# Performance work log

Measured on AMD Instinct MI355X. Metric: run time of the kernel, lower is better.

Reference implementation:

```python
import jax, jax.numpy as jnp
import numpy as np
import math

B, T, D, La, Lr = 8, 128, 512, 2, 2
H = La + Lr
DK = D // H  # 128
DFF = 4 * D


def _gelu(x):
    # BERT tanh-approx GELU, matching the torch module exactly
    return 0.5 * x * (1.0 + jnp.tanh(math.sqrt(2.0 / math.pi) * (x + 0.044715 * x ** 3)))


def _ln(x, g, b, eps=1e-5):
    mu = jnp.mean(x, axis=-1, keepdims=True)
    var = jnp.mean((x - mu) ** 2, axis=-1, keepdims=True)
    return (x - mu) * jax.lax.rsqrt(var + eps) * g + b


def setup_inputs() -> dict:
    key = jax.random.key(0)
    ks = jax.random.split(key, 16)
    n = lambda k, s, sc=1.0: jax.random.normal(k, s, dtype=jnp.float32) * sc
    return {
        'x': n(ks[0], (B, T, D)),
        'mask': jnp.ones((B, 1, T, T), dtype=jnp.int32),
        'abs_kernel': n(ks[1], (La, B, T, D)),
        'rel_kernel': n(ks[2], (Lr, B, T, T, D)),
        'Wc': n(ks[3], (3, D, D), 0.02), 'bc': jnp.zeros((3, D), jnp.float32),
        'Wpq': n(ks[4], (La, D, DK), 0.02), 'bpq': jnp.zeros((La, DK), jnp.float32),
        'Wpk': n(ks[5], (La, D, DK), 0.02), 'bpk': jnp.zeros((La, DK), jnp.float32),
        'Wrk': n(ks[6], (Lr, D, DK), 0.02), 'brk': jnp.zeros((Lr, DK), jnp.float32),
        'rel_bias': n(ks[7], (Lr, DK), 0.02),
        'Wo': n(ks[8], (D, D), 0.02), 'bo': jnp.zeros((D,), jnp.float32),
        'W1': n(ks[9], (D, DFF), 0.02), 'b1': jnp.zeros((DFF,), jnp.float32),
        'W2': n(ks[10], (DFF, D), 0.02), 'b2': jnp.zeros((D,), jnp.float32),
        'ln1_g': jnp.ones((D,), jnp.float32), 'ln1_b': jnp.zeros((D,), jnp.float32),
        'ln2_g': jnp.ones((D,), jnp.float32), 'ln2_b': jnp.zeros((D,), jnp.float32),
    }


def _attention(h, mask, abs_kernel, rel_kernel, Wc, bc, Wpq, bpq, Wpk, bpk,
               Wrk, brk, rel_bias, Wo, bo):
    b, t = h.shape[0], h.shape[1]
    # content projections: [3,B,T,D] -> [3,B,H,T,DK]
    qkv = jnp.einsum('btd,cde->cbte', h, Wc) + bc[:, None, None, :]
    qkv = qkv.reshape(3, b, t, H, DK).transpose(0, 1, 3, 2, 4)
    q, k, v = qkv[0], qkv[1], qkv[2]
    # absolute-position heads
    Pq = jnp.einsum('abtd,ade->bate', abs_kernel, Wpq) + bpq[None, :, None, :]
    Pk = jnp.einsum('abtd,ade->bate', abs_kernel, Wpk) + bpk[None, :, None, :]
    abs_scores = jnp.einsum('blid,bljd->blij', q[:, :La] + Pq, k[:, :La] + Pk)
    # relative-position heads (R: [B,Lr,T,T,DK])
    R = jnp.einsum('abijd,ade->baije', rel_kernel, Wrk) + brk[None, :, None, None, :]
    Xq = q[:, La:]
    rel_scores = jnp.einsum('blid,bljd->blij', Xq, k[:, La:])
    rel_scores = rel_scores + jnp.einsum('blid,blijd->blij', Xq + rel_bias[None, :, None, :], R)
    scores = jnp.concatenate([abs_scores, rel_scores], axis=1) * (DK ** -0.5)
    scores = jnp.where(mask == 0, jnp.float32(-1e9), scores)
    p_attn = jax.nn.softmax(scores, axis=-1)
    out = jnp.einsum('bhij,bhjd->bhid', p_attn, v)
    out = out.transpose(0, 2, 1, 3).reshape(b, t, H * DK)
    return out @ Wo + bo


def reference(x, mask, abs_kernel, rel_kernel, Wc, bc, Wpq, bpq, Wpk, bpk,
              Wrk, brk, rel_bias, Wo, bo, W1, b1, W2, b2,
              ln1_g, ln1_b, ln2_g, ln2_b):
    # pre-LN sublayer 1: attention
    h = _ln(x, ln1_g, ln1_b)
    x = x + _attention(h, mask, abs_kernel, rel_kernel, Wc, bc, Wpq, bpq,
                       Wpk, bpk, Wrk, brk, rel_bias, Wo, bo)
    # pre-LN sublayer 2: FFN with tanh-GELU
    h2 = _ln(x, ln2_g, ln2_b)
    x = x + (_gelu(h2 @ W1 + b1) @ W2 + b2)
    return x
```

## Files before the change

### kernel.cpp

```cpp
#include <hip/hip_runtime.h>
#include <math.h>

typedef __attribute__((ext_vector_type(8))) short short8v;
typedef __attribute__((ext_vector_type(4))) float f32x4;

static __device__ __forceinline__ ushort f2bf(float x) {
  unsigned u = __builtin_bit_cast(unsigned, x);
  unsigned r = (u + 0x7fffu + ((u >> 16) & 1u)) >> 16;
  return (ushort)r;
}

__device__ __forceinline__ float gelu_f(float v) {
  float t = tanhf(0.7978845608028654f * (v + 0.044715f * v * v * v));
  return 0.5f * v * (1.0f + t);
}

struct CvtTasks {
  const float* src[16];
  void* dst[16];
  int rows[16], cols[16], mode[16], aux[16], end[16];
};

__global__ __launch_bounds__(256) void cvt_kernel(CvtTasks T,
    const float* __restrict__ lnx, const float* __restrict__ lng,
    const float* __restrict__ lnb, ushort* __restrict__ lnout)
{
  __shared__ ushort tile[64][65];
  int b = blockIdx.x, t = threadIdx.x;
  int ti = 0;
  while (b >= T.end[ti]) ++ti;
  int lb = b - (ti ? T.end[ti-1] : 0);
  const float* src = T.src[ti];
  int mode = T.mode[ti];
  if (mode == 0) {
    int R = T.rows[ti], C = T.cols[ti];
    int tpr = C >> 6;
    int tyy = lb / tpr, txx = lb - tyy * tpr;
    int r0 = tyy << 6, c0 = txx << 6;
    int lr = t >> 4, lc4 = (t & 15) << 2;
    #pragma unroll
    for (int i = 0; i < 4; ++i) {
      int row = i*16 + lr;
      float4 vv = *(const float4*)(src + (size_t)(r0+row)*C + c0 + lc4);
      tile[row][lc4+0] = f2bf(vv.x);
      tile[row][lc4+1] = f2bf(vv.y);
      tile[row][lc4+2] = f2bf(vv.z);
      tile[row][lc4+3] = f2bf(vv.w);
    }
    __syncthreads();
    ushort* dst = (ushort*)T.dst[ti];
    #pragma unroll
    for (int i = 0; i < 4; ++i) {
      int n = i*16 + lr;
      ushort4 o;
      o.x = tile[lc4+0][n];
      o.y = tile[lc4+1][n];
      o.z = tile[lc4+2][n];
      o.w = tile[lc4+3][n];
      *(ushort4*)(dst + (size_t)(c0+n)*R + r0 + lc4) = o;
    }
  } else if (mode == 1) {
    int idx = lb*2048 + t*8;
    float4 v0 = *(const float4*)(src + idx);
    float4 v1 = *(const float4*)(src + idx + 4);
    union { ushort u[8]; uint4 q; } pk;
    pk.u[0]=f2bf(v0.x); pk.u[1]=f2bf(v0.y); pk.u[2]=f2bf(v0.z); pk.u[3]=f2bf(v0.w);
    pk.u[4]=f2bf(v1.x); pk.u[5]=f2bf(v1.y); pk.u[6]=f2bf(v1.z); pk.u[7]=f2bf(v1.w);
    *(uint4*)((ushort*)T.dst[ti] + idx) = pk.q;
  } else if (mode == 2) {
    if (t < T.cols[ti]) {
      float* d = (float*)T.dst[ti];
      for (int r = 0; r < T.rows[ti]; ++r)
        d[(size_t)(2*r + T.aux[ti]) * T.cols[ti] + t] = src[(size_t)r * T.cols[ti] + t];
    }
  } else {
    int row = lb*4 + (t >> 6);
    int lane = t & 63;
    const float* xr = lnx + (size_t)row*512 + lane*8;
    float4 a = *(const float4*)xr;
    float4 c = *(const float4*)(xr + 4);
    float s  = a.x + a.y + a.z + a.w + c.x + c.y + c.z + c.w;
    float ss = a.x*a.x + a.y*a.y + a.z*a.z + a.w*a.w
             + c.x*c.x + c.y*c.y + c.z*c.z + c.w*c.w;
    #pragma unroll
    for (int off = 32; off > 0; off >>= 1) {
      s  += __shfl_xor(s, off);
      ss += __shfl_xor(ss, off);
    }
    float mu  = s * (1.0f/512.0f);
    float var = ss * (1.0f/512.0f) - mu*mu;
    float rstd = rsqrtf(var + 1e-5f);
    float4 g0 = *(const float4*)(lng + lane*8), g1 = *(const float4*)(lng + lane*8 + 4);
    float4 b0 = *(const float4*)(lnb + lane*8), b1 = *(const float4*)(lnb + lane*8 + 4);
    union { ushort u[8]; uint4 v; } pk;
    pk.u[0] = f2bf((a.x-mu)*rstd*g0.x + b0.x);
    pk.u[1] = f2bf((a.y-mu)*rstd*g0.y + b0.y);
    pk.u[2] = f2bf((a.z-mu)*rstd*g0.z + b0.z);
    pk.u[3] = f2bf((a.w-mu)*rstd*g0.w + b0.w);
    pk.u[4] = f2bf((c.x-mu)*rstd*g1.x + b1.x);
    pk.u[5] = f2bf((c.y-mu)*rstd*g1.y + b1.y);
    pk.u[6] = f2bf((c.z-mu)*rstd*g1.z + b1.z);
    pk.u[7] = f2bf((c.w-mu)*rstd*g1.w + b1.w);
    *(uint4*)(lnout + (size_t)row*512 + lane*8) = pk.v;
  }
}

template<bool OUT_BF16, bool GELU_>
__device__ __forceinline__ void gemm64_body(
    const ushort* __restrict__ A, int lda,
    const ushort* __restrict__ Bt, int ldb,
    const float* __restrict__ bias,
    void* __restrict__ Cout, int ldc,
    int ksteps, int bm, int bn)
{
  __shared__ __align__(16) char smem[16384];
  char* asB = smem;
  char* bsB = smem + 8192;
  int tid = threadIdx.x;
  int lane = tid & 63, wid = tid >> 6;
  int wr = wid >> 1, wc = wid & 1;
  int l15 = lane & 15, kg = lane >> 4;
  f32x4 acc[2][2] = {};
  const ushort* Ab = A + (size_t)bm * lda;
  const ushort* Bb = Bt + (size_t)bn * ldb;
  int r0 = tid >> 3;
  int c16 = tid & 7;
  int wb0 = r0*128 + ((c16*16) ^ ((r0 & 7) << 4));
  int wb1 = (r0+32)*128 + ((c16*16) ^ ((r0 & 7) << 4));
  for (int ks = 0; ks < ksteps; ++ks) {
    int k0 = ks * 64;
    uint4 ra0 = *(const uint4*)(Ab + (size_t)r0*lda + k0 + c16*8);
    uint4 ra1 = *(const uint4*)(Ab + (size_t)(r0+32)*lda + k0 + c16*8);
    uint4 rb0 = *(const uint4*)(Bb + (size_t)r0*ldb + k0 + c16*8);
    uint4 rb1 = *(const uint4*)(Bb + (size_t)(r0+32)*ldb + k0 + c16*8);
    __syncthreads();
    *(uint4*)(asB + wb0) = ra0;  *(uint4*)(asB + wb1) = ra1;
    *(uint4*)(bsB + wb0) = rb0;  *(uint4*)(bsB + wb1) = rb1;
    __syncthreads();
    #pragma unroll
    for (int half = 0; half < 2; ++half) {
      int cb = half*64 + kg*16;
      short8v av[2], bv[2];
      #pragma unroll
      for (int m = 0; m < 2; ++m) {
        int r = wr*32 + m*16 + l15;
        av[m] = *(const short8v*)(asB + r*128 + (cb ^ ((r & 7) << 4)));
      }
      #pragma unroll
      for (int n = 0; n < 2; ++n) {
        int r = wc*32 + n*16 + l15;
        bv[n] = *(const short8v*)(bsB + r*128 + (cb ^ ((r & 7) << 4)));
      }
      #pragma unroll
      for (int m = 0; m < 2; ++m)
        #pragma unroll
        for (int n = 0; n < 2; ++n)
          acc[m][n] = __builtin_amdgcn_mfma_f32_16x16x32_bf16(av[m], bv[n], acc[m][n], 0, 0, 0);
    }
  }
  int orow0 = bm + wr*32 + kg*4;
  int ocol0 = bn + wc*32 + l15;
  #pragma unroll
  for (int m = 0; m < 2; ++m) {
    #pragma unroll
    for (int r = 0; r < 4; ++r) {
      int row = orow0 + m*16 + r;
      #pragma unroll
      for (int n = 0; n < 2; ++n) {
        int col = ocol0 + n*16;
        float val = acc[m][n][r];
        if (bias) val += bias[col];
        if (GELU_) val = gelu_f(val);
        if (OUT_BF16) ((ushort*)Cout)[(size_t)row*ldc + col] = f2bf(val);
        else          ((float*)Cout)[(size_t)row*ldc + col]  = val;
      }
    }
  }
}

template<bool OUT_BF16, bool GELU_>
__global__ __launch_bounds__(256) void g64(
    const ushort* __restrict__ A, int lda, long Abatch,
    const ushort* __restrict__ Bt, int ldb, long Bbatch,
    const float* __restrict__ bias, int biasStride,
    void* __restrict__ C, int ldc, long Cbatch,
    int ksteps)
{
  int z = blockIdx.z;
  const float* bz = bias ? bias + (size_t)z * biasStride : nullptr;
  void* Cz = OUT_BF16 ? (void*)((ushort*)C + (size_t)z*Cbatch)
                      : (void*)((float*)C + (size_t)z*Cbatch);
  gemm64_body<OUT_BF16, GELU_>(A + (size_t)z*Abatch, lda,
      Bt + (size_t)z*Bbatch, ldb, bz, Cz, ldc, ksteps,
      blockIdx.y*64, blockIdx.x*64);
}

__global__ __launch_bounds__(256) void qkvp_gemm(
    const ushort* __restrict__ h, const ushort* __restrict__ WcT,
    const float* __restrict__ bc, float* __restrict__ qkv,
    const ushort* __restrict__ absb, const ushort* __restrict__ Wp,
    const float* __restrict__ bqk, float* __restrict__ Pqk)
{
  int z = blockIdx.z;
  const ushort *A, *Bt;
  const float* bias;
  float* C;
  int ldc;
  if (z < 3) {
    A = h; Bt = WcT + (size_t)z*262144; bias = bc + z*512;
    C = qkv + (size_t)z*524288; ldc = 512;
  } else {
    if (blockIdx.x >= 2) return;
    int t = z - 3;
    A = absb + (size_t)(t >> 1)*524288;
    Bt = Wp + (size_t)t*65536;
    bias = bqk + t*128;
    C = Pqk + (size_t)t*131072; ldc = 128;
  }
  gemm64_body<false,false>(A, 512, Bt, 512, bias, C, ldc, 8,
      blockIdx.y*64, blockIdx.x*64);
}

__global__ __launch_bounds__(256) void fused_pre(
    const float* __restrict__ q, const float* __restrict__ k,
    float* __restrict__ Pqk, const float* __restrict__ rel_bias,
    const float* __restrict__ brk, const ushort* __restrict__ Wrkb,
    float* __restrict__ u, float* __restrict__ cvec)
{
  int blk = blockIdx.x;
  int tid = threadIdx.x;
  if (blk < 256) {
    int l = blk >> 7;
    int rem = blk & 127;
    int bm = (rem >> 3) * 64;
    int bn = (rem & 7) * 64;
    __shared__ __align__(16) char smem[16384];
    char* asB = smem;
    char* bsB = smem + 8192;
    int lane = tid & 63, wid = tid >> 6;
    int wr = wid >> 1, wc = wid & 1;
    int l15 = lane & 15, kg = lane >> 4;
    f32x4 acc[2][2] = {};
    const ushort* Bb = Wrkb + (size_t)l*65536 + (size_t)bn*128;
    int r0 = tid >> 3, c16 = tid & 7;
    int wb0 = r0*128 + ((c16*16) ^ ((r0 & 7) << 4));
    int wb1 = (r0+32)*128 + ((c16*16) ^ ((r0 & 7) << 4));
    const float* rbp = rel_bias + l*128;
    #pragma unroll
    for (int ks = 0; ks < 2; ++ks) {
      int k0 = ks * 64;
      int e0 = k0 + c16*8;
      uint4 ra[2], rb[2];
      #pragma unroll
      for (int i = 0; i < 2; ++i) {
        int m = bm + r0 + i*32;
        const float* qp = q + (size_t)m*512 + (2+l)*128 + e0;
        float4 qa = *(const float4*)qp;
        float4 qb = *(const float4*)(qp + 4);
        float4 rr0 = *(const float4*)(rbp + e0);
        float4 rr1 = *(const float4*)(rbp + e0 + 4);
        union { ushort s[8]; uint4 v; } pk;
        pk.s[0]=f2bf(qa.x+rr0.x); pk.s[1]=f2bf(qa.y+rr0.y);
        pk.s[2]=f2bf(qa.z+rr0.z); pk.s[3]=f2bf(qa.w+rr0.w);
        pk.s[4]=f2bf(qb.x+rr1.x); pk.s[5]=f2bf(qb.y+rr1.y);
        pk.s[6]=f2bf(qb.z+rr1.z); pk.s[7]=f2bf(qb.w+rr1.w);
        ra[i] = pk.v;
        rb[i] = *(const uint4*)(Bb + (size_t)(r0 + i*32)*128 + e0);
      }
      __syncthreads();
      *(uint4*)(asB + wb0) = ra[0];  *(uint4*)(asB + wb1) = ra[1];
      *(uint4*)(bsB + wb0) = rb[0];  *(uint4*)(bsB + wb1) = rb[1];
      __syncthreads();
      #pragma unroll
      for (int half = 0; half < 2; ++half) {
        int cb = half*64 + kg*16;
        short8v av[2], bv[2];
        #pragma unroll
        for (int m = 0; m < 2; ++m) {
          int r = wr*32 + m*16 + l15;
          av[m] = *(const short8v*)(asB + r*128 + (cb ^ ((r & 7) << 4)));
        }
        #pragma unroll
        for (int n = 0; n < 2; ++n) {
          int r = wc*32 + n*16 + l15;
          bv[n] = *(const short8v*)(bsB + r*128 + (cb ^ ((r & 7) << 4)));
        }
        #pragma unroll
        for (int m = 0; m < 2; ++m)
          #pragma unroll
          for (int n = 0; n < 2; ++n)
            acc[m][n] = __builtin_amdgcn_mfma_f32_16x16x32_bf16(av[m], bv[n], acc[m][n], 0, 0, 0);
      }
    }
    float* Cz = u + (size_t)l*524288;
    int orow0 = bm + wr*32 + kg*4;
    int ocol0 = bn + wc*32 + l15;
    #pragma unroll
    for (int m = 0; m < 2; ++m)
      #pragma unroll
      for (int r = 0; r < 4; ++r) {
        int row = orow0 + m*16 + r;
        #pragma unroll
        for (int n = 0; n < 2; ++n)
          Cz[(size_t)row*512 + ocol0 + n*16] = acc[m][n][r];
      }
  } else if (blk < 1280) {
    int idx = (blk - 256)*256 + tid;
    int dk = idx & 127;
    int rest = idx >> 7;
    int m = rest & 1023;
    int a = rest >> 10;
    Pqk[idx + a*131072]     += q[(size_t)m*512 + a*128 + dk];
    Pqk[idx + (a+1)*131072] += k[(size_t)m*512 + a*128 + dk];
  } else {
    int row = (blk - 1280)*2 + (tid >> 7);
    int l = row >> 10, m = row & 1023;
    int t = tid & 127, hf = tid >> 7;
    float val = q[(size_t)m*512 + (2+l)*128 + t] + rel_bias[l*128 + t];
    float p = brk[l*128 + t] * val;
    #pragma unroll
    for (int off = 32; off > 0; off >>= 1) p += __shfl_xor(p, off);
    __shared__ float red[2][2];
    if ((tid & 63) == 0) red[hf][(tid >> 6) & 1] = p;
    __syncthreads();
    if (t == 0) cvec[row] = red[hf][0] + red[hf][1];
  }
}

__global__ __launch_bounds__(256) void attn_kernel(
    const float* __restrict__ rk, const float* __restrict__ u,
    const float* __restrict__ q, const float* __restrict__ k,
    const float* __restrict__ v, const float* __restrict__ cvec,
    const float* __restrict__ Pqk, const int* __restrict__ mask,
    ushort* __restrict__ attnob)
{
  int blk = blockIdx.x;
  int tid = threadIdx.x;
  if (blk < 2048) {
    int i = blk & 127, b = (blk >> 7) & 7, l = blk >> 10, h = 2 + l;
    int m_i = b*128 + i;
    __shared__ float qs[128], sc[128], ps[128], red[64], pvs[2][128], stat[2];
    int wave = tid >> 6, lane = tid & 63;
    const float* ur = u + ((size_t)l*1024 + m_i)*512 + lane*8;
    float4 uu0 = *(const float4*)ur;
    float4 uu1 = *(const float4*)(ur + 4);
    if (tid < 128) qs[tid] = q[(size_t)m_i*512 + h*128 + tid];
    __syncthreads();
    float xq0 = qs[lane*2], xq1 = qs[lane*2+1];
    const float* base = rk + (size_t)blk*65536 + lane*8;
    const float* kb = k + (size_t)(b*128)*512 + h*128 + lane*2;
    #pragma unroll 2
    for (int jj = 0; jj < 32; ++jj) {
      int j = wave*32 + jj;
      const float* r = base + (size_t)j*512;
      float4 r0 = *(const float4*)r;
      float4 r1 = *(const float4*)(r + 4);
      float2 kk = *(const float2*)(kb + (size_t)j*512);
      float s = r0.x*uu0.x + r0.y*uu0.y + r0.z*uu0.z + r0.w*uu0.w
              + r1.x*uu1.x + r1.y*uu1.y + r1.z*uu1.z + r1.w*uu1.w
              + kk.x*xq0 + kk.y*xq1;
      #pragma unroll
      for (int off = 32; off > 0; off >>= 1) s += __shfl_xor(s, off);
      if (lane == 0) sc[j] = s;
    }
    __syncthreads();
    if (tid < 128) {
      float sv = (sc[tid] + cvec[l*1024 + m_i]) * 0.088388347648318447f;
      if (mask[((size_t)(b*128) + i)*128 + tid] == 0) sv = -1e9f;
      sc[tid] = sv;
    }
    __syncthreads();
    if (tid < 64) red[tid] = fmaxf(sc[tid], sc[tid+64]);
    __syncthreads();
    if (tid < 64) {
      float m = red[tid];
      #pragma unroll
      for (int off = 32; off > 0; off >>= 1) m = fmaxf(m, __shfl_xor(m, off));
      if (tid == 0) stat[0] = m;
    }
    __syncthreads();
    if (tid < 128) ps[tid] = __expf(sc[tid] - stat[0]);
    __syncthreads();
    if (tid < 64) red[tid] = ps[tid] + ps[tid+64];
    __syncthreads();
    if (tid < 64) {
      float s = red[tid];
      #pragma unroll
      for (int off = 32; off > 0; off >>= 1) s += __shfl_xor(s, off);
      if (tid == 0) stat[1] = 1.0f / s;
    }
    __syncthreads();
    int hf = tid >> 7, dk = tid & 127;
    const float* vp = v + (size_t)(b*128 + hf*64)*512 + h*128 + dk;
    float o = 0.0f;
    #pragma unroll 4
    for (int jj = 0; jj < 64; ++jj) o += ps[hf*64 + jj] * vp[(size_t)jj*512];
    pvs[hf][dk] = o;
    __syncthreads();
    if (tid < 128)
      attnob[(size_t)m_i*512 + h*128 + tid] = f2bf((pvs[0][tid] + pvs[1][tid]) * stat[1]);
  } else {
    int ab = blk - 2048;
    int hf = tid >> 7, t = tid & 127;
    int i  = (ab & 63)*2 + hf;
    int bh = ab >> 6;
    int h  = bh & 1, b = bh >> 1;
    __shared__ float qsh[2][128], psh[2][128], redm[2][2], reds[2][2];
    int m_i = b*128 + i;
    qsh[hf][t] = Pqk[(size_t)(2*h)*131072 + (size_t)m_i*128 + t];
    __syncthreads();
    int m_j = b*128 + t;
    const float* krow = Pqk + (size_t)(2*h+1)*131072 + (size_t)m_j*128;
    float dot = 0.0f;
    #pragma unroll
    for (int d = 0; d < 128; d += 4) {
      float4 kv = *(const float4*)(krow + d);
      dot += kv.x*qsh[hf][d] + kv.y*qsh[hf][d+1] + kv.z*qsh[hf][d+2] + kv.w*qsh[hf][d+3];
    }
    float s = dot * 0.088388347648318447f;
    if (mask[((size_t)(b*128) + i)*128 + t] == 0) s = -1e9f;
    float mx = s;
    #pragma unroll
    for (int off = 32; off > 0; off >>= 1) mx = fmaxf(mx, __shfl_xor(mx, off));
    int w2 = (tid >> 6) & 1;
    if ((tid & 63) == 0) redm[hf][w2] = mx;
    __syncthreads();
    mx = fmaxf(redm[hf][0], redm[hf][1]);
    float e = __expf(s - mx);
    psh[hf][t] = e;
    float sum = e;
    #pragma unroll
    for (int off = 32; off > 0; off >>= 1) sum += __shfl_xor(sum, off);
    if ((tid & 63) == 0) reds[hf][w2] = sum;
    __syncthreads();
    float inv = 1.0f / (reds[hf][0] + reds[hf][1]);
    const float* vp = v + (size_t)b*65536 + h*128 + t;
    float o = 0.0f;
    #pragma unroll 4
    for (int jj = 0; jj < 128; ++jj) o += psh[hf][jj] * vp[(size_t)jj*512];
    attnob[(size_t)m_i*512 + h*128 + t] = f2bf(o * inv);
  }
}

__global__ __launch_bounds__(256) void reduce_ln_kernel(
    const float* __restrict__ wpart, const float* __restrict__ bo,
    const float* __restrict__ x, const float* __restrict__ g,
    const float* __restrict__ bb, float* __restrict__ x1,
    ushort* __restrict__ h2)
{
  int gid = blockIdx.x*256 + threadIdx.x;
  int row = gid >> 6, lane = threadIdx.x & 63;
  size_t off = (size_t)row*512 + lane*8;
  float4 a = *(const float4*)(x + off);
  float4 c = *(const float4*)(x + off + 4);
  #pragma unroll
  for (int sk = 0; sk < 4; ++sk) {
    float4 p0 = *(const float4*)(wpart + (size_t)sk*524288 + off);
    float4 p1 = *(const float4*)(wpart + (size_t)sk*524288 + off + 4);
    a.x += p0.x; a.y += p0.y; a.z += p0.z; a.w += p0.w;
    c.x += p1.x; c.y += p1.y; c.z += p1.z; c.w += p1.w;
  }
  float4 bo0 = *(const float4*)(bo + lane*8);
  float4 bo1 = *(const float4*)(bo + lane*8 + 4);
  a.x += bo0.x; a.y += bo0.y; a.z += bo0.z; a.w += bo0.w;
  c.x += bo1.x; c.y += bo1.y; c.z += bo1.z; c.w += bo1.w;
  *(float4*)(x1 + off) = a;
  *(float4*)(x1 + off + 4) = c;
  float s  = a.x + a.y + a.z + a.w + c.x + c.y + c.z + c.w;
  float ss = a.x*a.x + a.y*a.y + a.z*a.z + a.w*a.w
           + c.x*c.x + c.y*c.y + c.z*c.z + c.w*c.w;
  #pragma unroll
  for (int off2 = 32; off2 > 0; off2 >>= 1) {
    s  += __shfl_xor(s, off2);
    ss += __shfl_xor(ss, off2);
  }
  float mu  = s * (1.0f/512.0f);
  float var = ss * (1.0f/512.0f) - mu*mu;
  float rstd = rsqrtf(var + 1e-5f);
  float4 g0 = *(const float4*)(g + lane*8), g1 = *(const float4*)(g + lane*8 + 4);
  float4 b0 = *(const float4*)(bb + lane*8), b1 = *(const float4*)(bb + lane*8 + 4);
  union { ushort u[8]; uint4 v; } pk;
  pk.u[0] = f2bf((a.x-mu)*rstd*g0.x + b0.x);
  pk.u[1] = f2bf((a.y-mu)*rstd*g0.y + b0.y);
  pk.u[2] = f2bf((a.z-mu)*rstd*g0.z + b0.z);
  pk.u[3] = f2bf((a.w-mu)*rstd*g0.w + b0.w);
  pk.u[4] = f2bf((c.x-mu)*rstd*g1.x + b1.x);
  pk.u[5] = f2bf((c.y-mu)*rstd*g1.y + b1.y);
  pk.u[6] = f2bf((c.z-mu)*rstd*g1.z + b1.z);
  pk.u[7] = f2bf((c.w-mu)*rstd*g1.w + b1.w);
  *(uint4*)(h2 + off) = pk.v;
}

__global__ __launch_bounds__(256) void reduce_out_kernel(
    const float* __restrict__ fpart, const float* __restrict__ b2,
    const float* __restrict__ x1, float* __restrict__ out)
{
  int idx = blockIdx.x*256 + threadIdx.x;
  size_t o4 = (size_t)idx*4;
  float4 s = *(const float4*)(x1 + o4);
  #pragma unroll
  for (int sk = 0; sk < 4; ++sk) {
    float4 p = *(const float4*)(fpart + (size_t)sk*524288 + o4);
    s.x += p.x; s.y += p.y; s.z += p.z; s.w += p.w;
  }
  float4 bv = *(const float4*)(b2 + ((idx & 127)*4));
  s.x += bv.x; s.y += bv.y; s.z += bv.z; s.w += bv.w;
  *(float4*)(out + o4) = s;
}

extern "C" void kernel_launch(void* const* d_in, const int* in_sizes, int n_in,
                              void* d_out, int out_size, void* d_ws, size_t ws_size,
                              hipStream_t stream)
{
  const float* x         = (const float*)d_in[0];
  const int*   mask      = (const int*)  d_in[1];
  const float* abs_kernel= (const float*)d_in[2];
  const float* rel_kernel= (const float*)d_in[3];
  const float* Wc        = (const float*)d_in[4];
  const float* bc        = (const float*)d_in[5];
  const float* Wpq       = (const float*)d_in[6];
  const float* bpq       = (const float*)d_in[7];
  const float* Wpk       = (const float*)d_in[8];
  const float* bpk       = (const float*)d_in[9];
  const float* Wrk       = (const float*)d_in[10];
  const float* brk       = (const float*)d_in[11];
  const float* rel_bias  = (const float*)d_in[12];
  const float* Wo        = (const float*)d_in[13];
  const float* bo        = (const float*)d_in[14];
  const float* W1        = (const float*)d_in[15];
  const float* b1        = (const float*)d_in[16];
  const float* W2        = (const float*)d_in[17];
  const float* b2        = (const float*)d_in[18];
  const float* ln1g      = (const float*)d_in[19];
  const float* ln1b      = (const float*)d_in[20];
  const float* ln2g      = (const float*)d_in[21];
  const float* ln2b      = (const float*)d_in[22];

  float* ws = (float*)d_ws;
  float* q      = ws;
  float* kbuf   = ws + 524288;
  float* v      = ws + 1048576;
  float* Pqk    = ws + 1572864;
  float* u      = ws + 2097152;
  float* x1     = ws + 3145728;
  float* cvec   = ws + 3670016;
  float* bqk    = ws + 3672064;
  float* wpart  = ws + 3672576;
  float* fpart  = wpart;
  ushort* bf    = (ushort*)(ws + 5769728);
  ushort* h     = bf;
  ushort* h2    = bf + 524288;
  ushort* attnob= bf + 1048576;
  ushort* f1    = bf + 1572864;
  ushort* absb  = bf + 3670016;
  ushort* WcT   = bf + 4718592;
  ushort* Wp    = bf + 5505024;
  ushort* Wrkb  = bf + 5767168;
  ushort* WoT   = bf + 5898240;
  ushort* W1T   = bf + 6160384;
  ushort* W2T   = bf + 7208960;
  float* out    = (float*)d_out;

  CvtTasks T{};
  int nb = 0, ti = 0;
  auto addTr = [&](const float* s, ushort* d, int R, int C) {
    T.src[ti]=s; T.dst[ti]=d; T.rows[ti]=R; T.cols[ti]=C; T.mode[ti]=0; T.aux[ti]=0;
    nb += (R/64)*(C/64); T.end[ti]=nb; ++ti;
  };
  auto addCv = [&](const float* s, ushort* d, int n) {
    T.src[ti]=s; T.dst[ti]=d; T.rows[ti]=n; T.cols[ti]=0; T.mode[ti]=1; T.aux[ti]=0;
    nb += n/2048; T.end[ti]=nb; ++ti;
  };
  auto addBi = [&](const float* s, float* d, int aux) {
    T.src[ti]=s; T.dst[ti]=d; T.rows[ti]=2; T.cols[ti]=128; T.mode[ti]=2; T.aux[ti]=aux;
    nb += 1; T.end[ti]=nb; ++ti;
  };
  for (int c = 0; c < 3; ++c) addTr(Wc + (size_t)c*262144, WcT + (size_t)c*262144, 512, 512);
  addTr(Wo, WoT, 512, 512);
  addTr(W1, W1T, 512, 2048);
  addTr(W2, W2T, 2048, 512);
  for (int a = 0; a < 2; ++a) addTr(Wpq + (size_t)a*65536, Wp + (size_t)(2*a)*65536, 512, 128);
  for (int a = 0; a < 2; ++a) addTr(Wpk + (size_t)a*65536, Wp + (size_t)(2*a+1)*65536, 512, 128);
  addCv(abs_kernel, absb, 1048576);
  addCv(Wrk, Wrkb, 131072);
  addBi(bpq, bqk, 0);
  addBi(bpk, bqk, 1);
  T.src[ti]=x; T.dst[ti]=h; T.mode[ti]=3; nb += 256; T.end[ti]=nb; ++ti;

  cvt_kernel<<<nb, 256, 0, stream>>>(T, x, ln1g, ln1b, h);

  qkvp_gemm<<<dim3(8,16,7), 256, 0, stream>>>(h, WcT, bc, q, absb, Wp, bqk, Pqk);

  fused_pre<<<2304, 256, 0, stream>>>(q, kbuf, Pqk, rel_bias, brk, Wrkb, u, cvec);

  attn_kernel<<<3072, 256, 0, stream>>>(rel_kernel, u, q, kbuf, v, cvec, Pqk, mask, attnob);

  g64<false,false><<<dim3(8,16,4), 256, 0, stream>>>(
      attnob, 512, 128, WoT, 512, 128, nullptr, 0, wpart, 512, 524288, 2);

  reduce_ln_kernel<<<256, 256, 0, stream>>>(wpart, bo, x, ln2g, ln2b, x1, h2);

  g64<true,true><<<dim3(32,16,1), 256, 0, stream>>>(
      h2, 512, 0, W1T, 512, 0, b1, 0, f1, 2048, 0, 8);

  g64<false,false><<<dim3(8,16,4), 256, 0, stream>>>(
      f1, 2048, 512, W2T, 2048, 512, nullptr, 0, fpart, 512, 524288, 8);

  reduce_out_kernel<<<512, 256, 0, stream>>>(fpart, b2, x1, out);
}
```

Before: 204.8 us.

## Merge pre-attention and post-attention kernel chains into persistent kernels with grid barriers

Replaces the QKV/positional GEMM plus fused_pre launches with one 512-block kernel, and the Wo GEMM, LN, FFN GEMMs and reductions with another. Phases inside each kernel are separated by an atomic-counter grid barrier, and the counters are reset in cvt_kernel. This removes several kernel launches and their inter-kernel gaps. In exchange it relies on all 512 blocks being co-resident (launch_bounds 256,2) and adds spin-wait barrier overhead.

```diff
diff --git a/kernel.cpp b/kernel.cpp
--- a/kernel.cpp
+++ b/kernel.cpp
@@ -13,6 +13,17 @@
 __device__ __forceinline__ float gelu_f(float v) {
   float t = tanhf(0.7978845608028654f * (v + 0.044715f * v * v * v));
   return 0.5f * v * (1.0f + t);
+}
+
+__device__ __forceinline__ void gbar(int* cnt, int target) {
+  __syncthreads();
+  if (threadIdx.x == 0) {
+    __hip_atomic_fetch_add(cnt, 1, __ATOMIC_RELEASE, __HIP_MEMORY_SCOPE_AGENT);
+    while (__hip_atomic_load(cnt, __ATOMIC_ACQUIRE, __HIP_MEMORY_SCOPE_AGENT) < target) {
+      __builtin_amdgcn_s_sleep(2);
+    }
+  }
+  __syncthreads();
 }
 
 struct CvtTasks {
@@ -23,8 +34,10 @@
 
 __global__ __launch_bounds__(256) void cvt_kernel(CvtTasks T,
     const float* __restrict__ lnx, const float* __restrict__ lng,
-    const float* __restrict__ lnb, ushort* __restrict__ lnout)
+    const float* __restrict__ lnb, ushort* __restrict__ lnout,
+    int* __restrict__ bars)
 {
+  if (blockIdx.x == 0 && threadIdx.x == 0) { bars[0] = 0; bars[1] = 0; }
   __shared__ ushort tile[64][65];
   int b = blockIdx.x, t = threadIdx.x;
   int ti = 0;
@@ -106,14 +119,13 @@
 }
 
 template<bool OUT_BF16, bool GELU_>
-__device__ __forceinline__ void gemm64_body(
+__device__ __forceinline__ void gemm64_body(char* smem,
     const ushort* __restrict__ A, int lda,
     const ushort* __restrict__ Bt, int ldb,
     const float* __restrict__ bias,
     void* __restrict__ Cout, int ldc,
     int ksteps, int bm, int bn)
 {
-  __shared__ __align__(16) char smem[16384];
   char* asB = smem;
   char* bsB = smem + 8192;
   int tid = threadIdx.x;
@@ -178,152 +190,134 @@
   }
 }
 
-template<bool OUT_BF16, bool GELU_>
-__global__ __launch_bounds__(256) void g64(
-    const ushort* __restrict__ A, int lda, long Abatch,
-    const ushort* __restrict__ Bt, int ldb, long Bbatch,
-    const float* __restrict__ bias, int biasStride,
-    void* __restrict__ C, int ldc, long Cbatch,
-    int ksteps)
-{
-  int z = blockIdx.z;
-  const float* bz = bias ? bias + (size_t)z * biasStride : nullptr;
-  void* Cz = OUT_BF16 ? (void*)((ushort*)C + (size_t)z*Cbatch)
-                      : (void*)((float*)C + (size_t)z*Cbatch);
-  gemm64_body<OUT_BF16, GELU_>(A + (size_t)z*Abatch, lda,
-      Bt + (size_t)z*Bbatch, ldb, bz, Cz, ldc, ksteps,
-      blockIdx.y*64, blockIdx.x*64);
-}
-
-__global__ __launch_bounds__(256) void qkvp_gemm(
+__global__ __launch_bounds__(256, 2) void mega1(
     const ushort* __restrict__ h, const ushort* __restrict__ WcT,
     const float* __restrict__ bc, float* __restrict__ qkv,
     const ushort* __restrict__ absb, const ushort* __restrict__ Wp,
-    const float* __restrict__ bqk, float* __restrict__ Pqk)
+    const float* __restrict__ bqk, float* __restrict__ Pqk,
+    const float* __restrict__ rel_bias, const float* __restrict__ brk,
+    const ushort* __restrict__ Wrkb, float* __restrict__ u,
+    float* __restrict__ cvec, int* __restrict__ bars)
 {
-  int z = blockIdx.z;
-  const ushort *A, *Bt;
-  const float* bias;
-  float* C;
-  int ldc;
-  if (z < 3) {
-    A = h; Bt = WcT + (size_t)z*262144; bias = bc + z*512;
-    C = qkv + (size_t)z*524288; ldc = 512;
-  } else {
-    if (blockIdx.x >= 2) return;
-    int t = z - 3;
-    A = absb + (size_t)(t >> 1)*524288;
-    Bt = Wp + (size_t)t*65536;
-    bias = bqk + t*128;
-    C = Pqk + (size_t)t*131072; ldc = 128;
-  }
-  gemm64_body<false,false>(A, 512, Bt, 512, bias, C, ldc, 8,
-      blockIdx.y*64, blockIdx.x*64);
-}
-
-__global__ __launch_bounds__(256) void fused_pre(
-    const float* __restrict__ q, const float* __restrict__ k,
-    float* __restrict__ Pqk, const float* __restrict__ rel_bias,
-    const float* __restrict__ brk, const ushort* __restrict__ Wrkb,
-    float* __restrict__ u, float* __restrict__ cvec)
-{
+  __shared__ __align__(16) char smem[16384];
   int blk = blockIdx.x;
   int tid = threadIdx.x;
-  if (blk < 256) {
-    int l = blk >> 7;
-    int rem = blk & 127;
-    int bm = (rem >> 3) * 64;
-    int bn = (rem & 7) * 64;
-    __shared__ __align__(16) char smem[16384];
-    char* asB = smem;
-    char* bsB = smem + 8192;
-    int lane = tid & 63, wid = tid >> 6;
-    int wr = wid >> 1, wc = wid & 1;
-    int l15 = lane & 15, kg = lane >> 4;
-    f32x4 acc[2][2] = {};
-    const ushort* Bb = Wrkb + (size_t)l*65536 + (size_t)bn*128;
-    int r0 = tid >> 3, c16 = tid & 7;
-    int wb0 = r0*128 + ((c16*16) ^ ((r0 & 7) << 4));
-    int wb1 = (r0+32)*128 + ((c16*16) ^ ((r0 & 7) << 4));
-    const float* rbp = rel_bias + l*128;
-    #pragma unroll
-    for (int ks = 0; ks < 2; ++ks) {
-      int k0 = ks * 64;
-      int e0 = k0 + c16*8;
-      uint4 ra[2], rb[2];
-      #pragma unroll
-      for (int i = 0; i < 2; ++i) {
-        int m = bm + r0 + i*32;
-        const float* qp = q + (size_t)m*512 + (2+l)*128 + e0;
-        float4 qa = *(const float4*)qp;
-        float4 qb = *(const float4*)(qp + 4);
-        float4 rr0 = *(const float4*)(rbp + e0);
-        float4 rr1 = *(const float4*)(rbp + e0 + 4);
-        union { ushort s[8]; uint4 v; } pk;
-        pk.s[0]=f2bf(qa.x+rr0.x); pk.s[1]=f2bf(qa.y+rr0.y);
-        pk.s[2]=f2bf(qa.z+rr0.z); pk.s[3]=f2bf(qa.w+rr0.w);
-        pk.s[4]=f2bf(qb.x+rr1.x); pk.s[5]=f2bf(qb.y+rr1.y);
-        pk.s[6]=f2bf(qb.z+rr1.z); pk.s[7]=f2bf(qb.w+rr1.w);
-        ra[i] = pk.v;
-        rb[i] = *(const uint4*)(Bb + (size_t)(r0 + i*32)*128 + e0);
+
+  if (blk < 384) {
+    int z = blk >> 7, rem = blk & 127;
+    int bn = (rem & 7) * 64, bm = (rem >> 3) * 64;
+    gemm64_body<false,false>(smem, h, 512, WcT + (size_t)z*262144, 512,
+        bc + z*512, qkv + (size_t)z*524288, 512, 8, bm, bn);
+  } else {
+    int t2 = blk - 384;
+    int z = t2 >> 5, rem = t2 & 31;
+    int bn = (rem & 1) * 64, bm = (rem >> 1) * 64;
+    gemm64_body<false,false>(smem, absb + (size_t)(z >> 1)*524288, 512,
+        Wp + (size_t)z*65536, 512, bqk + z*128,
+        Pqk + (size_t)z*131072, 128, 8, bm, bn);
+  }
+
+  gbar(bars, 512);
+
+  const float* q = qkv;
+  const float* k = qkv + 524288;
+  for (int t = blk; t < 2304; t += 512) {
+    if (t < 256) {
+      int l = t >> 7;
+      int rem = t & 127;
+      int bm = (rem >> 3) * 64;
+      int bn = (rem & 7) * 64;
+      char* asB = smem;
+      char* bsB = smem + 8192;
+      int lane = tid & 63, wid = tid >> 6;
+      int wr = wid >> 1, wc = wid & 1;
+      int l15 = lane & 15, kg = lane >> 4;
+      f32x4 acc[2][2] = {};
+      const ushort* Bb = Wrkb + (size_t)l*65536 + (size_t)bn*128;
+      int r0 = tid >> 3, c16 = tid & 7;
+      int wb0 = r0*128 + ((c16*16) ^ ((r0 & 7) << 4));
+      int wb1 = (r0+32)*128 + ((c16*16) ^ ((r0 & 7) << 4));
+      const float* rbp = rel_bias + l*128;
+      #pragma unroll
+      for (int ks = 0; ks < 2; ++ks) {
+        int k0 = ks * 64;
+        uint4 ra[2], rb[2];
+        #pragma unroll
+        for (int i = 0; i < 2; ++i) {
+          int m = bm + r0 + i*32;
+          int e0 = k0 + c16*8;
+          const float* qp = q + (size_t)m*512 + (2+l)*128 + e0;
+          float4 qa = *(const float4*)qp;
+          float4 qb = *(const float4*)(qp + 4);
+          float4 rr0 = *(const float4*)(rbp + e0);
+          float4 rr1 = *(const float4*)(rbp + e0 + 4);
+          union { ushort s[8]; uint4 v; } pk;
+          pk.s[0]=f2bf(qa.x+rr0.x); pk.s[1]=f2bf(qa.y+rr0.y);
+          pk.s[2]=f2bf(qa.z+rr0.z); pk.s[3]=f2bf(qa.w+rr0.w);
+          pk.s[4]=f2bf(qb.x+rr1.x); pk.s[5]=f2bf(qb.y+rr1.y);
+          pk.s[6]=f2bf(qb.z+rr1.z); pk.s[7]=f2bf(qb.w+rr1.w);
+          ra[i] = pk.v;
+          rb[i] = *(const uint4*)(Bb + (size_t)(r0 + i*32)*128 + k0 + c16*8);
+        }
+        __syncthreads();
+        *(uint4*)(asB + wb0) = ra[0];  *(uint4*)(asB + wb1) = ra[1];
+        *(uint4*)(bsB + wb0) = rb[0];  *(uint4*)(bsB + wb1) = rb[1];
+        __syncthreads();
+        #pragma unroll
+        for (int half = 0; half < 2; ++half) {
+          int cb = half*64 + kg*16;
+          short8v av[2], bv[2];
+          #pragma unroll
+          for (int m = 0; m < 2; ++m) {
+            int r = wr*32 + m*16 + l15;
+            av[m] = *(const short8v*)(asB + r*128 + (cb ^ ((r & 7) << 4)));
+          }
+          #pragma unroll
+          for (int n = 0; n < 2; ++n) {
+            int r = wc*32 + n*16 + l15;
+            bv[n] = *(const short8v*)(bsB + r*128 + (cb ^ ((r & 7) << 4)));
+          }
+          #pragma unroll
+          for (int m = 0; m < 2; ++m)
+            #pragma unroll
+            for (int n = 0; n < 2; ++n)
+              acc[m][n] = __builtin_amdgcn_mfma_f32_16x16x32_bf16(av[m], bv[n], acc[m][n], 0, 0, 0);
+        }
       }
-      __syncthreads();
-      *(uint4*)(asB + wb0) = ra[0];  *(uint4*)(asB + wb1) = ra[1];
-      *(uint4*)(bsB + wb0) = rb[0];  *(uint4*)(bsB + wb1) = rb[1];
-      __syncthreads();
-      #pragma unroll
-      for (int half = 0; half < 2; ++half) {
-        int cb = half*64 + kg*16;
-        short8v av[2], bv[2];
+      float* Cz = u + (size_t)l*524288;
+      int orow0 = bm + wr*32 + kg*4;
+      int ocol0 = bn + wc*32 + l15;
+      #pragma unroll
+      for (int m = 0; m < 2; ++m)
         #pragma unroll
-        for (int m = 0; m < 2; ++m) {
-          int r = wr*32 + m*16 + l15;
-          av[m] = *(const short8v*)(asB + r*128 + (cb ^ ((r & 7) << 4)));
-        }
-        #pragma unroll
-        for (int n = 0; n < 2; ++n) {
-          int r = wc*32 + n*16 + l15;
-          bv[n] = *(const short8v*)(bsB + r*128 + (cb ^ ((r & 7) << 4)));
-        }
-        #pragma unroll
-        for (int m = 0; m < 2; ++m)
+        for (int r = 0; r < 4; ++r) {
+          int row = orow0 + m*16 + r;
           #pragma unroll
           for (int n = 0; n < 2; ++n)
-            acc[m][n] = __builtin_amdgcn_mfma_f32_16x16x32_bf16(av[m], bv[n], acc[m][n], 0, 0, 0);
-      }
-    }
-    float* Cz = u + (size_t)l*524288;
-    int orow0 = bm + wr*32 + kg*4;
-    int ocol0 = bn + wc*32 + l15;
-    #pragma unroll
-    for (int m = 0; m < 2; ++m)
-      #pragma unroll
-      for (int r = 0; r < 4; ++r) {
-        int row = orow0 + m*16 + r;
-        #pragma unroll
-        for (int n = 0; n < 2; ++n)
-          Cz[(size_t)row*512 + ocol0 + n*16] = acc[m][n][r];
-      }
-  } else if (blk < 1280) {
-    int idx = (blk - 256)*256 + tid;
-    int dk = idx & 127;
-    int rest = idx >> 7;
-    int m = rest & 1023;
-    int a = rest >> 10;
-    Pqk[idx + a*131072]     += q[(size_t)m*512 + a*128 + dk];
-    Pqk[idx + (a+1)*131072] += k[(size_t)m*512 + a*128 + dk];
-  } else {
-    int row = (blk - 1280)*2 + (tid >> 7);
-    int l = row >> 10, m = row & 1023;
-    int t = tid & 127, hf = tid >> 7;
-    float val = q[(size_t)m*512 + (2+l)*128 + t] + rel_bias[l*128 + t];
-    float p = brk[l*128 + t] * val;
-    #pragma unroll
-    for (int off = 32; off > 0; off >>= 1) p += __shfl_xor(p, off);
-    __shared__ float red[2][2];
-    if ((tid & 63) == 0) red[hf][(tid >> 6) & 1] = p;
-    __syncthreads();
-    if (t == 0) cvec[row] = red[hf][0] + red[hf][1];
+            Cz[(size_t)row*512 + ocol0 + n*16] = acc[m][n][r];
+        }
+    } else if (t < 1280) {
+      int idx = (t - 256)*256 + tid;
+      int dk = idx & 127;
+      int rest = idx >> 7;
+      int m = rest & 1023;
+      int a = rest >> 10;
+      Pqk[idx + a*131072]     += q[(size_t)m*512 + a*128 + dk];
+      Pqk[idx + (a+1)*131072] += k[(size_t)m*512 + a*128 + dk];
+    } else {
+      int row = (t - 1280)*2 + (tid >> 7);
+      int l = row >> 10, m = row & 1023;
+      int tt = tid & 127, hf = tid >> 7;
+      float val = q[(size_t)m*512 + (2+l)*128 + tt] + rel_bias[l*128 + tt];
+      float p = brk[l*128 + tt] * val;
+      #pragma unroll
+      for (int off = 32; off > 0; off >>= 1) p += __shfl_xor(p, off);
+      __shared__ float red[2][2];
+      if ((tid & 63) == 0) red[hf][(tid >> 6) & 1] = p;
+      __syncthreads();
+      if (tt == 0) cvec[row] = red[hf][0] + red[hf][1];
+      __syncthreads();
+    }
   }
 }
 
@@ -442,70 +436,103 @@
   }
 }
 
-__global__ __launch_bounds__(256) void reduce_ln_kernel(
-    const float* __restrict__ wpart, const float* __restrict__ bo,
-    const float* __restrict__ x, const float* __restrict__ g,
-    const float* __restrict__ bb, float* __restrict__ x1,
-    ushort* __restrict__ h2)
+__global__ __launch_bounds__(256, 2) void mega2(
+    const ushort* __restrict__ attnob, const ushort* __restrict__ WoT,
+    float* __restrict__ wpart, const float* __restrict__ bo,
+    const float* __restrict__ x, const float* __restrict__ ln2g,
+    const float* __restrict__ ln2b, float* __restrict__ x1,
+    ushort* __restrict__ h2, const ushort* __restrict__ W1T,
+    const float* __restrict__ b1, ushort* __restrict__ f1,
+    const ushort* __restrict__ W2T, float* __restrict__ fpart,
+    const float* __restrict__ b2, float* __restrict__ out,
+    int* __restrict__ bars)
 {
-  int gid = blockIdx.x*256 + threadIdx.x;
-  int row = gid >> 6, lane = threadIdx.x & 63;
-  size_t off = (size_t)row*512 + lane*8;
-  float4 a = *(const float4*)(x + off);
-  float4 c = *(const float4*)(x + off + 4);
-  #pragma unroll
-  for (int sk = 0; sk < 4; ++sk) {
-    float4 p0 = *(const float4*)(wpart + (size_t)sk*524288 + off);
-    float4 p1 = *(const float4*)(wpart + (size_t)sk*524288 + off + 4);
-    a.x += p0.x; a.y += p0.y; a.z += p0.z; a.w += p0.w;
-    c.x += p1.x; c.y += p1.y; c.z += p1.z; c.w += p1.w;
-  }
-  float4 bo0 = *(const float4*)(bo + lane*8);
-  float4 bo1 = *(const float4*)(bo + lane*8 + 4);
-  a.x += bo0.x; a.y += bo0.y; a.z += bo0.z; a.w += bo0.w;
-  c.x += bo1.x; c.y += bo1.y; c.z += bo1.z; c.w += bo1.w;
-  *(float4*)(x1 + off) = a;
-  *(float4*)(x1 + off + 4) = c;
-  float s  = a.x + a.y + a.z + a.w + c.x + c.y + c.z + c.w;
-  float ss = a.x*a.x + a.y*a.y + a.z*a.z + a.w*a.w
-           + c.x*c.x + c.y*c.y + c.z*c.z + c.w*c.w;
-  #pragma unroll
-  for (int off2 = 32; off2 > 0; off2 >>= 1) {
-    s  += __shfl_xor(s, off2);
-    ss += __shfl_xor(ss, off2);
-  }
-  float mu  = s * (1.0f/512.0f);
-  float var = ss * (1.0f/512.0f) - mu*mu;
-  float rstd = rsqrtf(var + 1e-5f);
-  float4 g0 = *(const float4*)(g + lane*8), g1 = *(const float4*)(g + lane*8 + 4);
-  float4 b0 = *(const float4*)(bb + lane*8), b1 = *(const float4*)(bb + lane*8 + 4);
-  union { ushort u[8]; uint4 v; } pk;
-  pk.u[0] = f2bf((a.x-mu)*rstd*g0.x + b0.x);
-  pk.u[1] = f2bf((a.y-mu)*rstd*g0.y + b0.y);
-  pk.u[2] = f2bf((a.z-mu)*rstd*g0.z + b0.z);
-  pk.u[3] = f2bf((a.w-mu)*rstd*g0.w + b0.w);
-  pk.u[4] = f2bf((c.x-mu)*rstd*g1.x + b1.x);
-  pk.u[5] = f2bf((c.y-mu)*rstd*g1.y + b1.y);
-  pk.u[6] = f2bf((c.z-mu)*rstd*g1.z + b1.z);
-  pk.u[7] = f2bf((c.w-mu)*rstd*g1.w + b1.w);
-  *(uint4*)(h2 + off) = pk.v;
-}
-
-__global__ __launch_bounds__(256) void reduce_out_kernel(
-    const float* __restrict__ fpart, const float* __restrict__ b2,
-    const float* __restrict__ x1, float* __restrict__ out)
-{
-  int idx = blockIdx.x*256 + threadIdx.x;
-  size_t o4 = (size_t)idx*4;
-  float4 s = *(const float4*)(x1 + o4);
-  #pragma unroll
-  for (int sk = 0; sk < 4; ++sk) {
-    float4 p = *(const float4*)(fpart + (size_t)sk*524288 + o4);
-    s.x += p.x; s.y += p.y; s.z += p.z; s.w += p.w;
-  }
-  float4 bv = *(const float4*)(b2 + ((idx & 127)*4));
-  s.x += bv.x; s.y += bv.y; s.z += bv.z; s.w += bv.w;
-  *(float4*)(out + o4) = s;
+  __shared__ __align__(16) char smem[16384];
+  int blk = blockIdx.x;
+  int tid = threadIdx.x;
+
+  {
+    int z = blk >> 7, rem = blk & 127;
+    int bn = (rem & 7) * 64, bm = (rem >> 3) * 64;
+    gemm64_body<false,false>(smem, attnob + (size_t)z*128, 512,
+        WoT + (size_t)z*128, 512, nullptr,
+        wpart + (size_t)z*524288, 512, 2, bm, bn);
+  }
+  gbar(bars, 512);
+
+  if (blk < 256) {
+    int gid = blk*256 + tid;
+    int row = gid >> 6, lane = tid & 63;
+    size_t off = (size_t)row*512 + lane*8;
+    float4 a = *(const float4*)(x + off);
+    float4 c = *(const float4*)(x + off + 4);
+    #pragma unroll
+    for (int sk = 0; sk < 4; ++sk) {
+      float4 p0 = *(const float4*)(wpart + (size_t)sk*524288 + off);
+      float4 p1 = *(const float4*)(wpart + (size_t)sk*524288 + off + 4);
+      a.x += p0.x; a.y += p0.y; a.z += p0.z; a.w += p0.w;
+      c.x += p1.x; c.y += p1.y; c.z += p1.z; c.w += p1.w;
+    }
+    float4 bo0 = *(const float4*)(bo + lane*8);
+    float4 bo1 = *(const float4*)(bo + lane*8 + 4);
+    a.x += bo0.x; a.y += bo0.y; a.z += bo0.z; a.w += bo0.w;
+    c.x += bo1.x; c.y += bo1.y; c.z += bo1.z; c.w += bo1.w;
+    *(float4*)(x1 + off) = a;
+    *(float4*)(x1 + off + 4) = c;
+    float s  = a.x + a.y + a.z + a.w + c.x + c.y + c.z + c.w;
+    float ss = a.x*a.x + a.y*a.y + a.z*a.z + a.w*a.w
+             + c.x*c.x + c.y*c.y + c.z*c.z + c.w*c.w;
+    #pragma unroll
+    for (int off2 = 32; off2 > 0; off2 >>= 1) {
+      s  += __shfl_xor(s, off2);
+      ss += __shfl_xor(ss, off2);
+    }
+    float mu  = s * (1.0f/512.0f);
+    float var = ss * (1.0f/512.0f) - mu*mu;
+    float rstd = rsqrtf(var + 1e-5f);
+    float4 g0 = *(const float4*)(ln2g + lane*8), g1 = *(const float4*)(ln2g + lane*8 + 4);
+    float4 b0 = *(const float4*)(ln2b + lane*8), b1v = *(const float4*)(ln2b + lane*8 + 4);
+    union { ushort u[8]; uint4 v; } pk;
+    pk.u[0] = f2bf((a.x-mu)*rstd*g0.x + b0.x);
+    pk.u[1] = f2bf((a.y-mu)*rstd*g0.y + b0.y);
+    pk.u[2] = f2bf((a.z-mu)*rstd*g0.z + b0.z);
+    pk.u[3] = f2bf((a.w-mu)*rstd*g0.w + b0.w);
+    pk.u[4] = f2bf((c.x-mu)*rstd*g1.x + b1v.x);
+    pk.u[5] = f2bf((c.y-mu)*rstd*g1.y + b1v.y);
+    pk.u[6] = f2bf((c.z-mu)*rstd*g1.z + b1v.z);
+    pk.u[7] = f2bf((c.w-mu)*rstd*g1.w + b1v.w);
+    *(uint4*)(h2 + off) = pk.v;
+  }
+  gbar(bars, 1024);
+
+  {
+    int bn = (blk & 31) * 64, bm = (blk >> 5) * 64;
+    gemm64_body<true,true>(smem, h2, 512, W1T, 512, b1, f1, 2048, 8, bm, bn);
+  }
+  gbar(bars, 1536);
+
+  {
+    int z = blk >> 7, rem = blk & 127;
+    int bn = (rem & 7) * 64, bm = (rem >> 3) * 64;
+    gemm64_body<false,false>(smem, f1 + (size_t)z*512, 2048,
+        W2T + (size_t)z*512, 2048, nullptr,
+        fpart + (size_t)z*524288, 512, 8, bm, bn);
+  }
+  gbar(bars, 2048);
+
+  {
+    int idx = blk*256 + tid;
+    size_t o4 = (size_t)idx*4;
+    float4 s = *(const float4*)(x1 + o4);
+    #pragma unroll
+    for (int sk = 0; sk < 4; ++sk) {
+      float4 p = *(const float4*)(fpart + (size_t)sk*524288 + o4);
+      s.x += p.x; s.y += p.y; s.z += p.z; s.w += p.w;
+    }
+    float4 bv = *(const float4*)(b2 + ((idx & 127)*4));
+    s.x += bv.x; s.y += bv.y; s.z += bv.z; s.w += bv.w;
+    *(float4*)(out + o4) = s;
+  }
 }
 
 extern "C" void kernel_launch(void* const* d_in, const int* in_sizes, int n_in,
@@ -545,9 +572,10 @@
   float* x1     = ws + 3145728;
   float* cvec   = ws + 3670016;
   float* bqk    = ws + 3672064;
-  float* wpart  = ws + 3672576;
+  int*   bars   = (int*)(ws + 3672576);
+  float* wpart  = ws + 3672592;
   float* fpart  = wpart;
-  ushort* bf    = (ushort*)(ws + 5769728);
+  ushort* bf    = (ushort*)(ws + 5769760);
   ushort* h     = bf;
   ushort* h2    = bf + 524288;
   ushort* attnob= bf + 1048576;
@@ -587,24 +615,14 @@
   addBi(bpk, bqk, 1);
   T.src[ti]=x; T.dst[ti]=h; T.mode[ti]=3; nb += 256; T.end[ti]=nb; ++ti;
 
-  cvt_kernel<<<nb, 256, 0, stream>>>(T, x, ln1g, ln1b, h);
-
-  qkvp_gemm<<<dim3(8,16,7), 256, 0, stream>>>(h, WcT, bc, q, absb, Wp, bqk, Pqk);
-
-  fused_pre<<<2304, 256, 0, stream>>>(q, kbuf, Pqk, rel_bias, brk, Wrkb, u, cvec);
+  cvt_kernel<<<nb, 256, 0, stream>>>(T, x, ln1g, ln1b, h, bars);
+
+  mega1<<<512, 256, 0, stream>>>(h, WcT, bc, q, absb, Wp, bqk, Pqk,
+                                 rel_bias, brk, Wrkb, u, cvec, bars);
 
   attn_kernel<<<3072, 256, 0, stream>>>(rel_kernel, u, q, kbuf, v, cvec, Pqk, mask, attnob);
 
-  g64<false,false><<<dim3(8,16,4), 256, 0, stream>>>(
-      attnob, 512, 128, WoT, 512, 128, nullptr, 0, wpart, 512, 524288, 2);
-
-  reduce_ln_kernel<<<256, 256, 0, stream>>>(wpart, bo, x, ln2g, ln2b, x1, h2);
-
-  g64<true,true><<<dim3(32,16,1), 256, 0, stream>>>(
-      h2, 512, 0, W1T, 512, 0, b1, 0, f1, 2048, 0, 8);
-
-  g64<false,false><<<dim3(8,16,4), 256, 0, stream>>>(
-      f1, 2048, 512, W2T, 2048, 512, nullptr, 0, fpart, 512, 524288, 8);
-
-  reduce_out_kernel<<<512, 256, 0, stream>>>(fpart, b2, x1, out);
-}
+  mega2<<<512, 256, 0, stream>>>(attnob, WoT, wpart, bo, x, ln2g, ln2b,
+                                 x1, h2, W1T, b1, f1, W2T, fpart, b2, out,
+                                 bars + 1);
+}
```

Measured after the change: 419.7 us. 2.05x slower.
